# Kernel optimization log

Hardware: AMD Instinct MI355X
Metric: run time of the kernel (lower is better)

## Reference

```python
import math
import jax, jax.numpy as jnp
import numpy as np

N_NODES = 10000
N_EDGES = 160000
F_IN = 256
HID = 500
N_OUT = 100


def setup_inputs() -> dict:
    key = jax.random.key(0)
    ks = jax.random.split(key, 20)
    inp = {}
    inp['x'] = jax.random.normal(ks[0], (N_NODES, F_IN), jnp.float32)
    inp['edge_src'] = jax.random.randint(ks[1], (N_EDGES,), 0, N_NODES, jnp.int32)
    inp['edge_dst'] = jax.random.randint(ks[2], (N_EDGES,), 0, N_NODES, jnp.int32)
    inp['edge_weight'] = jax.random.uniform(ks[3], (N_EDGES,), jnp.float32)
    s1 = 1.0 / math.sqrt(F_IN)
    s2 = 1.0 / math.sqrt(HID)
    inp['W1_rel'] = jax.random.uniform(ks[4], (HID, F_IN), jnp.float32, -s1, s1)
    inp['b1'] = jax.random.uniform(ks[5], (HID,), jnp.float32, -s1, s1)
    inp['W1_root'] = jax.random.uniform(ks[6], (HID, F_IN), jnp.float32, -s1, s1)
    inp['p1_w'] = jax.random.uniform(ks[7], (HID,), jnp.float32, -s2, s2)
    inp['W2_rel'] = jax.random.uniform(ks[8], (HID, HID), jnp.float32, -s2, s2)
    inp['b2'] = jax.random.uniform(ks[9], (HID,), jnp.float32, -s2, s2)
    inp['W2_root'] = jax.random.uniform(ks[10], (HID, HID), jnp.float32, -s2, s2)
    inp['p2_w'] = jax.random.uniform(ks[11], (HID,), jnp.float32, -s2, s2)
    s3 = 1.0 / math.sqrt(1000)
    inp['lin1_W'] = jax.random.uniform(ks[12], (2000, 1000), jnp.float32, -s3, s3)
    inp['lin1_b'] = jax.random.uniform(ks[13], (2000,), jnp.float32, -s3, s3)
    s4 = 1.0 / math.sqrt(2000)
    inp['lin2_W'] = jax.random.uniform(ks[14], (4000, 2000), jnp.float32, -s4, s4)
    inp['lin2_b'] = jax.random.uniform(ks[15], (4000,), jnp.float32, -s4, s4)
    s5 = 1.0 / math.sqrt(4000)
    inp['lin3_W'] = jax.random.uniform(ks[16], (N_OUT, 4000), jnp.float32, -s5, s5)
    inp['lin3_b'] = jax.random.uniform(ks[17], (N_OUT,), jnp.float32, -s5, s5)
    return inp


def graph_conv(x, src, dst, w, W_rel, b_rel, W_root):
    # PyG GraphConv: out_i = W_rel @ sum_{j->i} w_ji * x_j + b + W_root @ x_i
    msg = x[src] * w[:, None]                              # [E, F]
    agg = jax.ops.segment_sum(msg, dst, num_segments=x.shape[0])
    return agg @ W_rel.T + b_rel + x @ W_root.T


def topk_pool(x, src, dst, w, p_w, ratio=0.5):
    # PyG TopKPooling: score = tanh(x @ p / ||p||); keep top-k; scale x by score.
    N = x.shape[0]
    k = int(math.ceil(ratio * N))
    score = jnp.tanh((x @ p_w) / jnp.linalg.norm(p_w))
    vals, perm = jax.lax.top_k(score, k)
    x_new = x[perm] * vals[:, None]
    # keep fixed-size edge list; dropped edges get weight 0 and point to node 0
    new_idx = jnp.zeros((N,), jnp.int32).at[perm].set(jnp.arange(k, dtype=jnp.int32))
    mask = jnp.zeros((N,), bool).at[perm].set(True)
    keep = mask[src] & mask[dst]
    src_new = jnp.where(keep, new_idx[src], 0)
    dst_new = jnp.where(keep, new_idx[dst], 0)
    w_new = jnp.where(keep, w, 0.0)
    return x_new, src_new, dst_new, w_new


def readout(x):
    # global max pool + global mean pool over the single graph -> [1, 2F]
    return jnp.concatenate([jnp.max(x, 0, keepdims=True), jnp.mean(x, 0, keepdims=True)], axis=1)


def reference(x, edge_src, edge_dst, edge_weight,
              W1_rel, b1, W1_root, p1_w,
              W2_rel, b2, W2_root, p2_w,
              lin1_W, lin1_b, lin2_W, lin2_b, lin3_W, lin3_b):
    h = jax.nn.relu(graph_conv(x, edge_src, edge_dst, edge_weight, W1_rel, b1, W1_root))
    h, s1, d1, w1 = topk_pool(h, edge_src, edge_dst, edge_weight, p1_w)
    x1 = readout(h)
    h = jax.nn.relu(graph_conv(h, s1, d1, w1, W2_rel, b2, W2_root))
    h, _, _, _ = topk_pool(h, s1, d1, w1, p2_w)
    x2 = readout(h)
    z = x1 + x2                                            # [1, 1000]
    z = jax.nn.relu(z @ lin1_W.T + lin1_b)
    z = jax.nn.relu(z @ lin2_W.T + lin2_b)                 # dropout is identity at eval
    return jax.nn.sigmoid(z @ lin3_W.T + lin3_b)
```

## Files before the change

kernel.cpp:

```cpp
#include <hip/hip_runtime.h>
#include <hip/hip_bf16.h>
#include <math.h>

#define NN1   10000
#define NE    160000
#define FIN   256
#define HID   500
#define K1    5000
#define NN2   5000
#define K2    2500

#define CSR_OFFS   0u
#define CSR_POS    10008u
#define CSR_SRC    20008u
#define CSR_W      180008u
#define OFF_AGG    340016u
#define OFF_H      2900016u
#define OFF_XP2    (OFF_H + 2500000u)
#define OFF_XP1    7900016u
#define OFF_SC1    10400016u
#define OFF_RK1    10410016u
#define OFF_SC2    10420016u
#define OFF_RK2    10425016u
#define OFF_RO     10430016u
#define OFF_Z      10432016u
#define OFF_T1     10433016u
#define OFF_T2     10435016u
#define OFF_INV    10439016u
#define OFF_CNT    10439024u
#define OFF_PM     10449024u
#define OFF_PS     10481024u
#define WS_FLOATS  10513024u

#define RCHUNK 500
#define ROSLAB1 64
#define ROSLAB2 32
#define RORPB   79

__device__ inline unsigned f2ord(float f) {
    unsigned u = __float_as_uint(f);
    return (u & 0x80000000u) ? ~u : (u | 0x80000000u);
}
__device__ inline unsigned long long rkey(float s, int j) {
    return ((unsigned long long)f2ord(s) << 32) | (unsigned)(0xFFFFFFFFu - (unsigned)j);
}
__device__ inline unsigned short bf16rn(float f) {
    unsigned u = __float_as_uint(f);
    u += 0x7FFFu + ((u >> 16) & 1u);
    return (unsigned short)(u >> 16);
}

typedef __attribute__((ext_vector_type(8))) short short8;
typedef __attribute__((ext_vector_type(4))) float floatx4;


__global__ void k_norms(const float* __restrict__ p1, const float* __restrict__ p2,
                        float* __restrict__ out) {
    const float* p = blockIdx.x ? p2 : p1;
    __shared__ float red[256];
    float s = 0.f;
    for (int i = threadIdx.x; i < HID; i += 256) { float v = p[i]; s += v * v; }
    red[threadIdx.x] = s; __syncthreads();
    for (int w = 128; w > 0; w >>= 1) {
        if (threadIdx.x < w) red[threadIdx.x] += red[threadIdx.x + w];
        __syncthreads();
    }
    if (threadIdx.x == 0) out[blockIdx.x] = 1.0f / sqrtf(red[0]);
}

__global__ void k_hist(const int* __restrict__ dst, int* __restrict__ pos) {
    int e = blockIdx.x * 256 + threadIdx.x;
    if (e < NE) atomicAdd(&pos[dst[e]], 1);
}

__global__ __launch_bounds__(1024) void k_scan(const int* __restrict__ deg, int* __restrict__ offs) {
    __shared__ int tot[1024];
    int t = threadIdx.x;
    int base = t * 10;
    int loc[10]; int s = 0;
    #pragma unroll
    for (int q = 0; q < 10; ++q) {
        int v = (base + q < NN1) ? deg[base + q] : 0;
        loc[q] = s; s += v;
    }
    tot[t] = s; __syncthreads();
    for (int d = 1; d < 1024; d <<= 1) {
        int v = (t >= d) ? tot[t - d] : 0;
        __syncthreads();
        tot[t] += v;
        __syncthreads();
    }
    int excl = (t == 0) ? 0 : tot[t - 1];
    #pragma unroll
    for (int q = 0; q < 10; ++q)
        if (base + q < NN1) offs[base + q] = excl + loc[q];
    if (t == 1023) offs[NN1] = tot[1023];
}

__global__ void k_copyoff(const int* __restrict__ offs, int* __restrict__ pos) {
    int i = blockIdx.x * 256 + threadIdx.x;
    if (i < NN1) pos[i] = offs[i];
}

__global__ void k_fill(const int* __restrict__ src, const int* __restrict__ dst,
                       const float* __restrict__ w, int* __restrict__ pos,
                       int* __restrict__ csrc, float* __restrict__ cw) {
    int e = blockIdx.x * 256 + threadIdx.x;
    if (e >= NE) return;
    int slot = atomicAdd(&pos[dst[e]], 1);
    csrc[slot] = src[e];
    cw[slot] = w[e];
}

__global__ __launch_bounds__(256) void k_gather1(
    const float* __restrict__ x, const int* __restrict__ offs,
    const int* __restrict__ csrc, const float* __restrict__ cw,
    float* __restrict__ agg) {
    int wave = (blockIdx.x * 256 + threadIdx.x) >> 6;
    int lane = threadIdx.x & 63;
    if (wave >= NN1) return;
    int b = offs[wave], e = offs[wave + 1];
    float4 acc = make_float4(0.f, 0.f, 0.f, 0.f);
    for (int p = b; p < e; ++p) {
        int s = csrc[p]; float we = cw[p];
        float4 v = *(const float4*)(x + (size_t)s * FIN + lane * 4);
        acc.x += v.x * we; acc.y += v.y * we; acc.z += v.z * we; acc.w += v.w * we;
    }
    *(float4*)(agg + (size_t)wave * FIN + lane * 4) = acc;
}

__global__ __launch_bounds__(256) void k_gather2(
    const float* __restrict__ Xp, const int* __restrict__ offs,
    const int* __restrict__ csrc, const float* __restrict__ cw,
    const int* __restrict__ rank, float* __restrict__ agg) {
    int wave = (blockIdx.x * 256 + threadIdx.x) >> 6;
    int lane = threadIdx.x & 63;
    if (wave >= NN1) return;
    int rd = rank[wave];
    if (rd < 0) return;
    int b = offs[wave], e = offs[wave + 1];
    int c1 = 256 + lane * 4;
    float a0 = 0.f, a1 = 0.f, a2 = 0.f, a3 = 0.f;
    float b0 = 0.f, b1v = 0.f, b2 = 0.f, b3 = 0.f;
    for (int p = b; p < e; ++p) {
        int s = csrc[p];
        int rs = rank[s];
        if (rs < 0) continue;
        float we = cw[p];
        const float* row = Xp + (size_t)rs * HID;
        float4 v = *(const float4*)(row + lane * 4);
        a0 += v.x * we; a1 += v.y * we; a2 += v.z * we; a3 += v.w * we;
        if (c1 < HID) {
            float4 v2 = *(const float4*)(row + c1);
            b0 += v2.x * we; b1v += v2.y * we; b2 += v2.z * we; b3 += v2.w * we;
        }
    }
    float* o = agg + (size_t)rd * HID;
    *(float4*)(o + lane * 4) = make_float4(a0, a1, a2, a3);
    if (c1 < HID) *(float4*)(o + c1) = make_float4(b0, b1v, b2, b3);
}

#define GBK 32
#define APAD 40
__global__ __launch_bounds__(256) void k_gemm_mfma(
    const float* __restrict__ A1, const float* __restrict__ B1,
    const float* __restrict__ A2, const float* __restrict__ B2,
    const float* __restrict__ bias, float* __restrict__ C,
    int M, int N, int Ka, int Kb, int nbyRow) {
    int b = blockIdx.x;
    int xcd = b & 7, seq = b >> 3;
    int colT = seq & 7;
    int rowT = xcd + 8 * (seq >> 3);
    if (rowT >= nbyRow) return;
    int row0 = rowT * 64, col0 = colT * 64;

    __shared__ unsigned short As[64 * APAD];
    __shared__ unsigned short Bs[64 * APAD];
    int tid = threadIdx.x;
    int lane = tid & 63, wid = tid >> 6;
    int waveM = wid & 1, waveN = wid >> 1;
    int quad = lane >> 4, mrow = lane & 15;
    floatx4 acc[2][2] = {};

    int sr = tid >> 2;
    int sk = (tid & 3) * 8;

    int nka = (Ka + GBK - 1) / GBK;
    int nkb = (Kb + GBK - 1) / GBK;
    int niter = nka + nkb;

    float4 pa[2], pb[2];
    {
        int gr = row0 + sr, gn = col0 + sr;
        #pragma unroll
        for (int j = 0; j < 2; ++j) {
            int gk = sk + j * 4;
            pa[j] = (gr < M && gk < Ka) ? *(const float4*)(A1 + (size_t)gr * Ka + gk)
                                        : make_float4(0.f, 0.f, 0.f, 0.f);
            pb[j] = (gn < N && gk < Ka) ? *(const float4*)(B1 + (size_t)gn * Ka + gk)
                                        : make_float4(0.f, 0.f, 0.f, 0.f);
        }
    }

    for (int it = 0; it < niter; ++it) {
        {
            union { unsigned short us[8]; short8 v8; } ua, ub;
            #pragma unroll
            for (int j = 0; j < 2; ++j) {
                ua.us[j*4+0] = bf16rn(pa[j].x); ua.us[j*4+1] = bf16rn(pa[j].y);
                ua.us[j*4+2] = bf16rn(pa[j].z); ua.us[j*4+3] = bf16rn(pa[j].w);
                ub.us[j*4+0] = bf16rn(pb[j].x); ub.us[j*4+1] = bf16rn(pb[j].y);
                ub.us[j*4+2] = bf16rn(pb[j].z); ub.us[j*4+3] = bf16rn(pb[j].w);
            }
            *(short8*)&As[sr * APAD + sk] = ua.v8;
            *(short8*)&Bs[sr * APAD + sk] = ub.v8;
        }
        __syncthreads();
        if (it + 1 < niter) {
            int t = it + 1;
            int ph = (t >= nka);
            const float* A = ph ? A2 : A1;
            const float* B = ph ? B2 : B1;
            int K = ph ? Kb : Ka;
            int k0 = (ph ? t - nka : t) * GBK;
            int gr = row0 + sr, gn = col0 + sr;
            #pragma unroll
            for (int j = 0; j < 2; ++j) {
                int gk = k0 + sk + j * 4;
                pa[j] = (gr < M && gk < K) ? *(const float4*)(A + (size_t)gr * K + gk)
                                           : make_float4(0.f, 0.f, 0.f, 0.f);
                pb[j] = (gn < N && gk < K) ? *(const float4*)(B + (size_t)gn * K + gk)
                                           : make_float4(0.f, 0.f, 0.f, 0.f);
            }
        }
        short8 bfr[2];
        #pragma unroll
        for (int nt = 0; nt < 2; ++nt)
            bfr[nt] = *(short8*)&Bs[(waveN * 32 + nt * 16 + mrow) * APAD + quad * 8];
        #pragma unroll
        for (int mt = 0; mt < 2; ++mt) {
            short8 afr = *(short8*)&As[(waveM * 32 + mt * 16 + mrow) * APAD + quad * 8];
            #pragma unroll
            for (int nt = 0; nt < 2; ++nt)
                acc[mt][nt] = __builtin_amdgcn_mfma_f32_16x16x32_bf16(
                    afr, bfr[nt], acc[mt][nt], 0, 0, 0);
        }
        __syncthreads();
    }
    #pragma unroll
    for (int nt = 0; nt < 2; ++nt) {
        int col = col0 + waveN * 32 + nt * 16 + mrow;
        if (col >= N) continue;
        float bv = bias[col];
        #pragma unroll
        for (int mt = 0; mt < 2; ++mt) {
            int rbase = row0 + waveM * 32 + mt * 16 + quad * 4;
            #pragma unroll
            for (int r = 0; r < 4; ++r) {
                int row = rbase + r;
                if (row < M) C[(size_t)row * N + col] = fmaxf(acc[mt][nt][r] + bv, 0.f);
            }
        }
    }
}

__global__ __launch_bounds__(256) void k_scores(
    const float* __restrict__ H, const float* __restrict__ p,
    const float* __restrict__ invnorm, float* __restrict__ score, int Nn) {
    int wave = (blockIdx.x * 256 + threadIdx.x) >> 6;
    int lane = threadIdx.x & 63;
    if (wave >= Nn) return;
    const float* h = H + (size_t)wave * HID;
    float s = 0.f;
    for (int i = lane; i < HID; i += 64) s += h[i] * p[i];
    for (int off = 32; off > 0; off >>= 1) s += __shfl_down(s, off, 64);
    if (lane == 0) score[wave] = tanhf(s * invnorm[0]);
}

__global__ __launch_bounds__(256) void k_rank_partial(
    const float* __restrict__ score, int* __restrict__ cnt, int Nn) {
    __shared__ unsigned long long kj[RCHUNK];
    int j0 = blockIdx.y * RCHUNK;
    int jn = min(Nn - j0, RCHUNK);
    for (int t = threadIdx.x; t < jn; t += 256)
        kj[t] = rkey(score[j0 + t], j0 + t);
    __syncthreads();
    int i = blockIdx.x * 256 + threadIdx.x;
    if (i >= Nn) return;
    unsigned long long ki = rkey(score[i], i);
    int c = 0;
    #pragma unroll 4
    for (int q = 0; q < jn; ++q)
        c += (kj[q] > ki) ? 1 : 0;
    atomicAdd(&cnt[i], c);
}

__global__ void k_rank_final(const int* __restrict__ cnt, int* __restrict__ rank,
                             int Nn, int k) {
    int i = blockIdx.x * 256 + threadIdx.x;
    if (i < Nn) { int c = cnt[i]; rank[i] = (c < k) ? c : -1; }
}

__global__ __launch_bounds__(128) void k_gather(
    const float* __restrict__ H, const float* __restrict__ score,
    const int* __restrict__ rank, float* __restrict__ Xp) {
    int i = blockIdx.x;
    int r = rank[i];
    if (r < 0) return;
    float sc = score[i];
    int c = threadIdx.x;
    if (c < HID / 4) {
        float4 v = *(const float4*)(H + (size_t)i * HID + c * 4);
        v.x *= sc; v.y *= sc; v.z *= sc; v.w *= sc;
        *(float4*)(Xp + (size_t)r * HID + c * 4) = v;
    }
}

__global__ __launch_bounds__(256) void k_readout_slab(
    const float* __restrict__ X, int rows, int rpb,
    float* __restrict__ pmax, float* __restrict__ psum) {
    __shared__ float4 lmx[4][64];
    __shared__ float4 lsm[4][64];
    int lane = threadIdx.x & 63;
    int rgrp = threadIdx.x >> 6;
    int c4 = blockIdx.x * 64 + lane;
    int r0 = blockIdx.y * rpb;
    int r1 = min(rows, r0 + rpb);
    float4 mx = make_float4(-INFINITY, -INFINITY, -INFINITY, -INFINITY);
    float4 sm = make_float4(0.f, 0.f, 0.f, 0.f);
    if (c4 < HID / 4) {
        for (int r = r0 + rgrp; r < r1; r += 4) {
            float4 v = *(const float4*)(X + (size_t)r * HID + c4 * 4);
            mx.x = fmaxf(mx.x, v.x); mx.y = fmaxf(mx.y, v.y);
            mx.z = fmaxf(mx.z, v.z); mx.w = fmaxf(mx.w, v.w);
            sm.x += v.x; sm.y += v.y; sm.z += v.z; sm.w += v.w;
        }
    }
    lmx[rgrp][lane] = mx; lsm[rgrp][lane] = sm;
    __syncthreads();
    if (rgrp == 0 && c4 < HID / 4) {
        #pragma unroll
        for (int g = 1; g < 4; ++g) {
            float4 m2 = lmx[g][lane], s2 = lsm[g][lane];
            mx.x = fmaxf(mx.x, m2.x); mx.y = fmaxf(mx.y, m2.y);
            mx.z = fmaxf(mx.z, m2.z); mx.w = fmaxf(mx.w, m2.w);
            sm.x += s2.x; sm.y += s2.y; sm.z += s2.z; sm.w += s2.w;
        }
        *(float4*)(pmax + (size_t)blockIdx.y * HID + c4 * 4) = mx;
        *(float4*)(psum + (size_t)blockIdx.y * HID + c4 * 4) = sm;
    }
}

__global__ __launch_bounds__(64) void k_ro_final(
    const float* __restrict__ pmax, const float* __restrict__ psum, int nslab,
    float* __restrict__ fmax, float* __restrict__ fsum) {
    int j = blockIdx.x * 64 + threadIdx.x;
    if (j >= HID) return;
    float mx = -INFINITY, sm = 0.f;
    for (int s = 0; s < nslab; ++s) {
        mx = fmaxf(mx, pmax[(size_t)s * HID + j]);
        sm += psum[(size_t)s * HID + j];
    }
    fmax[j] = mx; fsum[j] = sm;
}

__global__ void k_combine(const float* __restrict__ m1, const float* __restrict__ s1,
                          const float* __restrict__ m2, const float* __restrict__ s2,
                          float* __restrict__ z) {
    int j = blockIdx.x * 256 + threadIdx.x;
    if (j >= 1000) return;
    float a, b;
    if (j < 500) { a = m1[j]; b = m2[j]; }
    else { a = s1[j - 500] * (1.0f / (float)K1); b = s2[j - 500] * (1.0f / (float)K2); }
    z[j] = a + b;
}

__global__ __launch_bounds__(256) void k_mv(
    const float* __restrict__ v, const float* __restrict__ W,
    const float* __restrict__ bias, float* __restrict__ y,
    int rowsN, int K, int act) {
    int wave = (blockIdx.x * 256 + threadIdx.x) >> 6;
    int lane = threadIdx.x & 63;
    if (wave >= rowsN) return;
    const float* wr = W + (size_t)wave * K;
    float s = 0.f;
    for (int c = lane * 4; c < K; c += 256) {
        float4 a = *(const float4*)(wr + c);
        float4 xv = *(const float4*)(v + c);
        s += a.x * xv.x + a.y * xv.y + a.z * xv.z + a.w * xv.w;
    }
    for (int off = 32; off > 0; off >>= 1) s += __shfl_down(s, off, 64);
    if (lane == 0) {
        float r = s + bias[wave];
        y[wave] = (act == 0) ? fmaxf(r, 0.f) : 1.f / (1.f + expf(-r));
    }
}

extern "C" void kernel_launch(void* const* d_in, const int* in_sizes, int n_in,
                              void* d_out, int out_size, void* d_ws, size_t ws_size,
                              hipStream_t stream) {
    const float* x      = (const float*)d_in[0];
    const int*   esrc   = (const int*)d_in[1];
    const int*   edst   = (const int*)d_in[2];
    const float* ew     = (const float*)d_in[3];
    const float* W1_rel = (const float*)d_in[4];
    const float* b1     = (const float*)d_in[5];
    const float* W1_root= (const float*)d_in[6];
    const float* p1     = (const float*)d_in[7];
    const float* W2_rel = (const float*)d_in[8];
    const float* b2     = (const float*)d_in[9];
    const float* W2_root= (const float*)d_in[10];
    const float* p2     = (const float*)d_in[11];
    const float* l1W    = (const float*)d_in[12];
    const float* l1b    = (const float*)d_in[13];
    const float* l2W    = (const float*)d_in[14];
    const float* l2b    = (const float*)d_in[15];
    const float* l3W    = (const float*)d_in[16];
    const float* l3b    = (const float*)d_in[17];
    float* out = (float*)d_out;
    float* ws  = (float*)d_ws;

    if (ws_size < (size_t)WS_FLOATS * sizeof(float)) return;

    int*      offs  = (int*)(ws + CSR_OFFS);
    int*      pos   = (int*)(ws + CSR_POS);
    int*      csrc  = (int*)(ws + CSR_SRC);
    float*    cw    = ws + CSR_W;
    float*    agg   = ws + OFF_AGG;
    float*    h     = ws + OFF_H;
    float*    xp1   = ws + OFF_XP1;
    float*    xp2   = ws + OFF_XP2;
    float*    sc1   = ws + OFF_SC1;
    int*      rk1   = (int*)(ws + OFF_RK1);
    float*    sc2   = ws + OFF_SC2;
    int*      rk2   = (int*)(ws + OFF_RK2);
    float*    max1  = ws + OFF_RO;
    float*    sum1  = ws + OFF_RO + 500;
    float*    max2  = ws + OFF_RO + 1000;
    float*    sum2  = ws + OFF_RO + 1500;
    float*    zbuf  = ws + OFF_Z;
    float*    t1    = ws + OFF_T1;
    float*    t2    = ws + OFF_T2;
    float*    invn  = ws + OFF_INV;
    int*      cnt   = (int*)(ws + OFF_CNT);
    float*    pmax  = ws + OFF_PM;
    float*    psum  = ws + OFF_PS;

    hipMemsetAsync(pos, 0, NN1 * sizeof(int), stream);

    k_norms<<<2, 256, 0, stream>>>(p1, p2, invn);

    k_hist<<<(NE + 255) / 256, 256, 0, stream>>>(edst, pos);
    k_scan<<<1, 1024, 0, stream>>>(pos, offs);
    k_copyoff<<<(NN1 + 255) / 256, 256, 0, stream>>>(offs, pos);
    k_fill<<<(NE + 255) / 256, 256, 0, stream>>>(esrc, edst, ew, pos, csrc, cw);

    k_gather1<<<(NN1 * 64 + 255) / 256, 256, 0, stream>>>(x, offs, csrc, cw, agg);
    {
        int nby = (NN1 + 63) / 64;
        int nblk = 64 * ((nby + 7) / 8);
        k_gemm_mfma<<<nblk, 256, 0, stream>>>(
            agg, W1_rel, x, W1_root, b1, h, NN1, HID, FIN, FIN, nby);
    }

    k_scores<<<(NN1 * 64 + 255) / 256, 256, 0, stream>>>(h, p1, invn + 0, sc1, NN1);
    hipMemsetAsync(cnt, 0, NN1 * sizeof(int), stream);
    k_rank_partial<<<dim3((NN1 + 255) / 256, NN1 / RCHUNK), 256, 0, stream>>>(sc1, cnt, NN1);
    k_rank_final<<<(NN1 + 255) / 256, 256, 0, stream>>>(cnt, rk1, NN1, K1);
    k_gather<<<NN1, 128, 0, stream>>>(h, sc1, rk1, xp1);
    k_readout_slab<<<dim3(2, ROSLAB1), 256, 0, stream>>>(xp1, K1, RORPB, pmax, psum);
    k_ro_final<<<(HID + 63) / 64, 64, 0, stream>>>(pmax, psum, ROSLAB1, max1, sum1);

    k_gather2<<<(NN1 * 64 + 255) / 256, 256, 0, stream>>>(xp1, offs, csrc, cw, rk1, agg);
    {
        int nby = (NN2 + 63) / 64;
        int nblk = 64 * ((nby + 7) / 8);
        k_gemm_mfma<<<nblk, 256, 0, stream>>>(
            agg, W2_rel, xp1, W2_root, b2, h, NN2, HID, HID, HID, nby);
    }

    k_scores<<<(NN2 * 64 + 255) / 256, 256, 0, stream>>>(h, p2, invn + 1, sc2, NN2);
    hipMemsetAsync(cnt, 0, NN2 * sizeof(int), stream);
    k_rank_partial<<<dim3((NN2 + 255) / 256, NN2 / RCHUNK), 256, 0, stream>>>(sc2, cnt, NN2);
    k_rank_final<<<(NN2 + 255) / 256, 256, 0, stream>>>(cnt, rk2, NN2, K2);
    k_gather<<<NN2, 128, 0, stream>>>(h, sc2, rk2, xp2);
    k_readout_slab<<<dim3(2, ROSLAB2), 256, 0, stream>>>(xp2, K2, RORPB, pmax, psum);
    k_ro_final<<<(HID + 63) / 64, 64, 0, stream>>>(pmax, psum, ROSLAB2, max2, sum2);

    k_combine<<<4, 256, 0, stream>>>(max1, sum1, max2, sum2, zbuf);
    k_mv<<<(2000 * 64) / 256, 256, 0, stream>>>(zbuf, l1W, l1b, t1, 2000, 1000, 0);
    k_mv<<<(4000 * 64) / 256, 256, 0, stream>>>(t1, l2W, l2b, t2, 4000, 2000, 0);
    k_mv<<<(100 * 64) / 256, 256, 0, stream>>>(t2, l3W, l3b, out, 100, 4000, 1);
}
```

Baseline: 381.9 us.

## Stage GEMM operands in bf16 so the MFMA GEMM skips in-loop conversion

A new batched conversion kernel turns x and the four GraphConv weight matrices into bf16 at the start of each call. The gather kernels now write their aggregates as bf16, and the pooling gather also writes a bf16 copy of the pooled features. The GEMM then loads bf16 directly, which halves its global and L2 load traffic and removes the per-iteration fp32-to-bf16 rounding in its main loop. In exchange there is an extra pass that reads and writes about 15 MB of x and weights per call, plus a larger workspace.

```diff
diff --git a/kernel.cpp b/kernel.cpp
--- a/kernel.cpp
+++ b/kernel.cpp
@@ -30,7 +30,13 @@
 #define OFF_CNT    10439024u
 #define OFF_PM     10449024u
 #define OFF_PS     10481024u
-#define WS_FLOATS  10513024u
+#define OFF_XB     10513024u
+#define OFF_W1RB   11793024u
+#define OFF_W1TB   11857024u
+#define OFF_W2RB   11921024u
+#define OFF_W2TB   12046024u
+#define OFF_XP1B   12171024u
+#define WS_FLOATS  13421024u
 
 #define RCHUNK 500
 #define ROSLAB1 64
@@ -51,6 +57,7 @@
 }
 
 typedef __attribute__((ext_vector_type(8))) short short8;
+typedef __attribute__((ext_vector_type(4))) short short4v;
 typedef __attribute__((ext_vector_type(4))) float floatx4;
 
 
@@ -68,6 +75,31 @@
     if (threadIdx.x == 0) out[blockIdx.x] = 1.0f / sqrtf(red[0]);
 }
 
+__global__ __launch_bounds__(256) void k_cvt5(
+    const float* __restrict__ s0, unsigned short* __restrict__ d0, int n0,
+    const float* __restrict__ s1, unsigned short* __restrict__ d1, int n1,
+    const float* __restrict__ s2, unsigned short* __restrict__ d2, int n2,
+    const float* __restrict__ s3, unsigned short* __restrict__ d3, int n3,
+    const float* __restrict__ s4, unsigned short* __restrict__ d4, int n4) {
+    const float* s; unsigned short* d; int n;
+    switch (blockIdx.y) {
+        case 0: s = s0; d = d0; n = n0; break;
+        case 1: s = s1; d = d1; n = n1; break;
+        case 2: s = s2; d = d2; n = n2; break;
+        case 3: s = s3; d = d3; n = n3; break;
+        default: s = s4; d = d4; n = n4; break;
+    }
+    int i = (blockIdx.x * 256 + threadIdx.x) * 4;
+    if (i + 3 >= n) {
+        for (int q = 0; q < 4 && i + q < n; ++q) d[i + q] = bf16rn(s[i + q]);
+        return;
+    }
+    float4 v = *(const float4*)(s + i);
+    ushort4 o;
+    o.x = bf16rn(v.x); o.y = bf16rn(v.y); o.z = bf16rn(v.z); o.w = bf16rn(v.w);
+    *(ushort4*)(d + i) = o;
+}
+
 __global__ void k_hist(const int* __restrict__ dst, int* __restrict__ pos) {
     int e = blockIdx.x * 256 + threadIdx.x;
     if (e < NE) atomicAdd(&pos[dst[e]], 1);
@@ -115,7 +147,7 @@
 __global__ __launch_bounds__(256) void k_gather1(
     const float* __restrict__ x, const int* __restrict__ offs,
     const int* __restrict__ csrc, const float* __restrict__ cw,
-    float* __restrict__ agg) {
+    unsigned short* __restrict__ aggb) {
     int wave = (blockIdx.x * 256 + threadIdx.x) >> 6;
     int lane = threadIdx.x & 63;
     if (wave >= NN1) return;
@@ -126,13 +158,15 @@
         float4 v = *(const float4*)(x + (size_t)s * FIN + lane * 4);
         acc.x += v.x * we; acc.y += v.y * we; acc.z += v.z * we; acc.w += v.w * we;
     }
-    *(float4*)(agg + (size_t)wave * FIN + lane * 4) = acc;
+    ushort4 o;
+    o.x = bf16rn(acc.x); o.y = bf16rn(acc.y); o.z = bf16rn(acc.z); o.w = bf16rn(acc.w);
+    *(ushort4*)(aggb + (size_t)wave * FIN + lane * 4) = o;
 }
 
 __global__ __launch_bounds__(256) void k_gather2(
     const float* __restrict__ Xp, const int* __restrict__ offs,
     const int* __restrict__ csrc, const float* __restrict__ cw,
-    const int* __restrict__ rank, float* __restrict__ agg) {
+    const int* __restrict__ rank, unsigned short* __restrict__ aggb) {
     int wave = (blockIdx.x * 256 + threadIdx.x) >> 6;
     int lane = threadIdx.x & 63;
     if (wave >= NN1) return;
@@ -155,16 +189,20 @@
             b0 += v2.x * we; b1v += v2.y * we; b2 += v2.z * we; b3 += v2.w * we;
         }
     }
-    float* o = agg + (size_t)rd * HID;
-    *(float4*)(o + lane * 4) = make_float4(a0, a1, a2, a3);
-    if (c1 < HID) *(float4*)(o + c1) = make_float4(b0, b1v, b2, b3);
+    unsigned short* o = aggb + (size_t)rd * HID;
+    ushort4 o1; o1.x = bf16rn(a0); o1.y = bf16rn(a1); o1.z = bf16rn(a2); o1.w = bf16rn(a3);
+    *(ushort4*)(o + lane * 4) = o1;
+    if (c1 < HID) {
+        ushort4 o2; o2.x = bf16rn(b0); o2.y = bf16rn(b1v); o2.z = bf16rn(b2); o2.w = bf16rn(b3);
+        *(ushort4*)(o + c1) = o2;
+    }
 }
 
 #define GBK 32
 #define APAD 40
-__global__ __launch_bounds__(256) void k_gemm_mfma(
-    const float* __restrict__ A1, const float* __restrict__ B1,
-    const float* __restrict__ A2, const float* __restrict__ B2,
+__global__ __launch_bounds__(256) void k_gemm_bf16(
+    const unsigned short* __restrict__ A1, const unsigned short* __restrict__ B1,
+    const unsigned short* __restrict__ A2, const unsigned short* __restrict__ B2,
     const float* __restrict__ bias, float* __restrict__ C,
     int M, int N, int Ka, int Kb, int nbyRow) {
     int b = blockIdx.x;
@@ -189,49 +227,44 @@
     int nkb = (Kb + GBK - 1) / GBK;
     int niter = nka + nkb;
 
-    float4 pa[2], pb[2];
-    {
-        int gr = row0 + sr, gn = col0 + sr;
-        #pragma unroll
-        for (int j = 0; j < 2; ++j) {
-            int gk = sk + j * 4;
-            pa[j] = (gr < M && gk < Ka) ? *(const float4*)(A1 + (size_t)gr * Ka + gk)
-                                        : make_float4(0.f, 0.f, 0.f, 0.f);
-            pb[j] = (gn < N && gk < Ka) ? *(const float4*)(B1 + (size_t)gn * Ka + gk)
-                                        : make_float4(0.f, 0.f, 0.f, 0.f);
-        }
-    }
+    short4v pa0 = {0,0,0,0}, pa1 = {0,0,0,0}, pb0 = {0,0,0,0}, pb1 = {0,0,0,0};
+
+    auto fetch = [&](const unsigned short* A, const unsigned short* B, int K, int k0) {
+        int gr = row0 + sr, gn = col0 + sr, gk = k0 + sk;
+        short4v z = {0,0,0,0};
+        pa0 = z; pa1 = z; pb0 = z; pb1 = z;
+        if (gr < M) {
+            const unsigned short* p = A + (size_t)gr * K + gk;
+            if (gk + 7 < K) { pa0 = *(const short4v*)p; pa1 = *(const short4v*)(p + 4); }
+            else {
+                unsigned short tmp[8] = {0,0,0,0,0,0,0,0};
+                for (int q = 0; q < 8; ++q) if (gk + q < K) tmp[q] = p[q];
+                pa0 = *(short4v*)&tmp[0]; pa1 = *(short4v*)&tmp[4];
+            }
+        }
+        if (gn < N) {
+            const unsigned short* p = B + (size_t)gn * K + gk;
+            if (gk + 7 < K) { pb0 = *(const short4v*)p; pb1 = *(const short4v*)(p + 4); }
+            else {
+                unsigned short tmp[8] = {0,0,0,0,0,0,0,0};
+                for (int q = 0; q < 8; ++q) if (gk + q < K) tmp[q] = p[q];
+                pb0 = *(short4v*)&tmp[0]; pb1 = *(short4v*)&tmp[4];
+            }
+        }
+    };
+
+    fetch(A1, B1, Ka, 0);
 
     for (int it = 0; it < niter; ++it) {
-        {
-            union { unsigned short us[8]; short8 v8; } ua, ub;
-            #pragma unroll
-            for (int j = 0; j < 2; ++j) {
-                ua.us[j*4+0] = bf16rn(pa[j].x); ua.us[j*4+1] = bf16rn(pa[j].y);
-                ua.us[j*4+2] = bf16rn(pa[j].z); ua.us[j*4+3] = bf16rn(pa[j].w);
-                ub.us[j*4+0] = bf16rn(pb[j].x); ub.us[j*4+1] = bf16rn(pb[j].y);
-                ub.us[j*4+2] = bf16rn(pb[j].z); ub.us[j*4+3] = bf16rn(pb[j].w);
-            }
-            *(short8*)&As[sr * APAD + sk] = ua.v8;
-            *(short8*)&Bs[sr * APAD + sk] = ub.v8;
-        }
+        *(short4v*)&As[sr * APAD + sk]     = pa0;
+        *(short4v*)&As[sr * APAD + sk + 4] = pa1;
+        *(short4v*)&Bs[sr * APAD + sk]     = pb0;
+        *(short4v*)&Bs[sr * APAD + sk + 4] = pb1;
         __syncthreads();
         if (it + 1 < niter) {
             int t = it + 1;
             int ph = (t >= nka);
-            const float* A = ph ? A2 : A1;
-            const float* B = ph ? B2 : B1;
-            int K = ph ? Kb : Ka;
-            int k0 = (ph ? t - nka : t) * GBK;
-            int gr = row0 + sr, gn = col0 + sr;
-            #pragma unroll
-            for (int j = 0; j < 2; ++j) {
-                int gk = k0 + sk + j * 4;
-                pa[j] = (gr < M && gk < K) ? *(const float4*)(A + (size_t)gr * K + gk)
-                                           : make_float4(0.f, 0.f, 0.f, 0.f);
-                pb[j] = (gn < N && gk < K) ? *(const float4*)(B + (size_t)gn * K + gk)
-                                           : make_float4(0.f, 0.f, 0.f, 0.f);
-            }
+            fetch(ph ? A2 : A1, ph ? B2 : B1, ph ? Kb : Ka, (ph ? t - nka : t) * GBK);
         }
         short8 bfr[2];
         #pragma unroll
@@ -303,7 +336,8 @@
 
 __global__ __launch_bounds__(128) void k_gather(
     const float* __restrict__ H, const float* __restrict__ score,
-    const int* __restrict__ rank, float* __restrict__ Xp) {
+    const int* __restrict__ rank, float* __restrict__ Xp,
+    unsigned short* __restrict__ Xb) {
     int i = blockIdx.x;
     int r = rank[i];
     if (r < 0) return;
@@ -313,6 +347,11 @@
         float4 v = *(const float4*)(H + (size_t)i * HID + c * 4);
         v.x *= sc; v.y *= sc; v.z *= sc; v.w *= sc;
         *(float4*)(Xp + (size_t)r * HID + c * 4) = v;
+        if (Xb) {
+            ushort4 o;
+            o.x = bf16rn(v.x); o.y = bf16rn(v.y); o.z = bf16rn(v.z); o.w = bf16rn(v.w);
+            *(ushort4*)(Xb + (size_t)r * HID + c * 4) = o;
+        }
     }
 }
 
@@ -422,68 +461,80 @@
 
     if (ws_size < (size_t)WS_FLOATS * sizeof(float)) return;
 
-    int*      offs  = (int*)(ws + CSR_OFFS);
-    int*      pos   = (int*)(ws + CSR_POS);
-    int*      csrc  = (int*)(ws + CSR_SRC);
-    float*    cw    = ws + CSR_W;
-    float*    agg   = ws + OFF_AGG;
-    float*    h     = ws + OFF_H;
-    float*    xp1   = ws + OFF_XP1;
-    float*    xp2   = ws + OFF_XP2;
-    float*    sc1   = ws + OFF_SC1;
-    int*      rk1   = (int*)(ws + OFF_RK1);
-    float*    sc2   = ws + OFF_SC2;
-    int*      rk2   = (int*)(ws + OFF_RK2);
-    float*    max1  = ws + OFF_RO;
-    float*    sum1  = ws + OFF_RO + 500;
-    float*    max2  = ws + OFF_RO + 1000;
-    float*    sum2  = ws + OFF_RO + 1500;
-    float*    zbuf  = ws + OFF_Z;
-    float*    t1    = ws + OFF_T1;
-    float*    t2    = ws + OFF_T2;
-    float*    invn  = ws + OFF_INV;
-    int*      cnt   = (int*)(ws + OFF_CNT);
-    float*    pmax  = ws + OFF_PM;
-    float*    psum  = ws + OFF_PS;
+    int*            offs  = (int*)(ws + CSR_OFFS);
+    int*            pos   = (int*)(ws + CSR_POS);
+    int*            csrc  = (int*)(ws + CSR_SRC);
+    float*          cw    = ws + CSR_W;
+    unsigned short* aggb  = (unsigned short*)(ws + OFF_AGG);
+    float*          h     = ws + OFF_H;
+    float*          xp1   = ws + OFF_XP1;
+    float*          xp2   = ws + OFF_XP2;
+    float*          sc1   = ws + OFF_SC1;
+    int*            rk1   = (int*)(ws + OFF_RK1);
+    float*          sc2   = ws + OFF_SC2;
+    int*            rk2   = (int*)(ws + OFF_RK2);
+    float*          max1  = ws + OFF_RO;
+    float*          sum1  = ws + OFF_RO + 500;
+    float*          max2  = ws + OFF_RO + 1000;
+    float*          sum2  = ws + OFF_RO + 1500;
+    float*          zbuf  = ws + OFF_Z;
+    float*          t1    = ws + OFF_T1;
+    float*          t2    = ws + OFF_T2;
+    float*          invn  = ws + OFF_INV;
+    int*            cnt   = (int*)(ws + OFF_CNT);
+    float*          pmax  = ws + OFF_PM;
+    float*          psum  = ws + OFF_PS;
+    unsigned short* xb    = (unsigned short*)(ws + OFF_XB);
+    unsigned short* w1rb  = (unsigned short*)(ws + OFF_W1RB);
+    unsigned short* w1tb  = (unsigned short*)(ws + OFF_W1TB);
+    unsigned short* w2rb  = (unsigned short*)(ws + OFF_W2RB);
+    unsigned short* w2tb  = (unsigned short*)(ws + OFF_W2TB);
+    unsigned short* xp1b  = (unsigned short*)(ws + OFF_XP1B);
 
     hipMemsetAsync(pos, 0, NN1 * sizeof(int), stream);
 
     k_norms<<<2, 256, 0, stream>>>(p1, p2, invn);
+    k_cvt5<<<dim3(2500, 5), 256, 0, stream>>>(
+        x, xb, NN1 * FIN,
+        W1_rel, w1rb, HID * FIN,
+        W1_root, w1tb, HID * FIN,
+        W2_rel, w2rb, HID * HID,
+        W2_root, w2tb, HID * HID);
 
     k_hist<<<(NE + 255) / 256, 256, 0, stream>>>(edst, pos);
     k_scan<<<1, 1024, 0, stream>>>(pos, offs);
     k_copyoff<<<(NN1 + 255) / 256, 256, 0, stream>>>(offs, pos);
     k_fill<<<(NE + 255) / 256, 256, 0, stream>>>(esrc, edst, ew, pos, csrc, cw);
 
-    k_gather1<<<(NN1 * 64 + 255) / 256, 256, 0, stream>>>(x, offs, csrc, cw, agg);
+    k_gather1<<<(NN1 * 64 + 255) / 256, 256, 0, stream>>>(x, offs, csrc, cw, aggb);
     {
         int nby = (NN1 + 63) / 64;
         int nblk = 64 * ((nby + 7) / 8);
-        k_gemm_mfma<<<nblk, 256, 0, stream>>>(
-            agg, W1_rel, x, W1_root, b1, h, NN1, HID, FIN, FIN, nby);
+        k_gemm_bf16<<<nblk, 256, 0, stream>>>(
+            aggb, w1rb, xb, w1tb, b1, h, NN1, HID, FIN, FIN, nby);
     }
 
     k_scores<<<(NN1 * 64 + 255) / 256, 256, 0, stream>>>(h, p1, invn + 0, sc1, NN1);
     hipMemsetAsync(cnt, 0, NN1 * sizeof(int), stream);
     k_rank_partial<<<dim3((NN1 + 255) / 256, NN1 / RCHUNK), 256, 0, stream>>>(sc1, cnt, NN1);
     k_rank_final<<<(NN1 + 255) / 256, 256, 0, stream>>>(cnt, rk1, NN1, K1);
-    k_gather<<<NN1, 128, 0, stream>>>(h, sc1, rk1, xp1);
+    k_gather<<<NN1, 128, 0, stream>>>(h, sc1, rk1, xp1, xp1b);
     k_readout_slab<<<dim3(2, ROSLAB1), 256, 0, stream>>>(xp1, K1, RORPB, pmax, psum);
     k_ro_final<<<(HID + 63) / 64, 64, 0, stream>>>(pmax, psum, ROSLAB1, max1, sum1);
 
-    k_gather2<<<(NN1 * 64 + 255) / 256, 256, 0, stream>>>(xp1, offs, csrc, cw, rk1, agg);
+    k_gather2<<<(NN1 * 64 + 255) / 256, 256, 0, stream>>>(xp1, offs, csrc, cw, rk1, aggb);
     {
         int nby = (NN2 + 63) / 64;
         int nblk = 64 * ((nby + 7) / 8);
-        k_gemm_mfma<<<nblk, 256, 0, stream>>>(
-            agg, W2_rel, xp1, W2_root, b2, h, NN2, HID, HID, HID, nby);
+        k_gemm_bf16<<<nblk, 256, 0, stream>>>(
+            aggb, w2rb, xp1b, w2tb, b2, h, NN2, HID, HID, HID, nby);
     }
 
     k_scores<<<(NN2 * 64 + 255) / 256, 256, 0, stream>>>(h, p2, invn + 1, sc2, NN2);
     hipMemsetAsync(cnt, 0, NN2 * sizeof(int), stream);
     k_rank_partial<<<dim3((NN2 + 255) / 256, NN2 / RCHUNK), 256, 0, stream>>>(sc2, cnt, NN2);
     k_rank_final<<<(NN2 + 255) / 256, 256, 0, stream>>>(cnt, rk2, NN2, K2);
-    k_gather<<<NN2, 128, 0, stream>>>(h, sc2, rk2, xp2);
+    k_gather<<<NN2, 128, 0, stream>>>(h, sc2, rk2, xp2, (unsigned short*)nullptr);
     k_readout_slab<<<dim3(2, ROSLAB2), 256, 0, stream>>>(xp2, K2, RORPB, pmax, psum);
     k_ro_final<<<(HID + 63) / 64, 64, 0, stream>>>(pmax, psum, ROSLAB2, max2, sum2);
 
```

Result: faster. 365.4 us (-4.3%).
